# Kernel tuning notes

Measured on AMD Instinct MI355X. Metric: run time of the kernel, lower is better.

## Reference

```python
import jax, jax.numpy as jnp
import numpy as np

B, N, D, H, NW = 16, 400, 256, 8, 4
DH = D // H
EPS_LN = 1e-5

def _layer_norm(x, g, b):
    m = jnp.mean(x, axis=-1, keepdims=True)
    v = jnp.mean((x - m) ** 2, axis=-1, keepdims=True)
    return (x - m) / jnp.sqrt(v + EPS_LN) * g + b

def setup_inputs() -> dict:
    key = jax.random.key(0)
    ks = jax.random.split(key, 10)
    p = lambda k, shape: (jax.random.normal(k, shape, jnp.float32) * 0.02)
    return {
        'x': jax.random.normal(ks[0], (B, N, D), jnp.float32),
        'attention_weights': jax.random.normal(ks[1], (B, NW, N, N), jnp.float32),
        'Wq': p(ks[2], (D, D)), 'bq': jnp.zeros((D,), jnp.float32),
        'Wk': p(ks[3], (D, D)), 'bk': jnp.zeros((D,), jnp.float32),
        'Wv': p(ks[4], (D, D)), 'bv': jnp.zeros((D,), jnp.float32),
        'Wo': p(ks[5], (D, D)), 'bo': jnp.zeros((D,), jnp.float32),
        'g1': jnp.ones((D,), jnp.float32), 'beta1': jnp.zeros((D,), jnp.float32),
        'W1': p(ks[6], (4 * D, D)), 'b1': jnp.zeros((4 * D,), jnp.float32),
        'W2': p(ks[7], (D, 4 * D)), 'b2': jnp.zeros((D,), jnp.float32),
        'g2': jnp.ones((D,), jnp.float32), 'beta2': jnp.zeros((D,), jnp.float32),
    }

def reference(x, attention_weights, Wq, bq, Wk, bk, Wv, bv, Wo, bo,
              g1, beta1, W1, b1, W2, b2, g2, beta2):
    b, n, d = x.shape
    # QKV projections, split heads: [B, H, N, DH]
    q = (x @ Wq.T + bq).reshape(b, n, H, DH).transpose(0, 2, 1, 3)
    k = (x @ Wk.T + bk).reshape(b, n, H, DH).transpose(0, 2, 1, 3)
    v = (x @ Wv.T + bv).reshape(b, n, H, DH).transpose(0, 2, 1, 3)
    qk = jnp.einsum('bhnd,bhmd->bhnm', q, k) / np.sqrt(DH)  # [B,H,N,N]
    # signed attention averaged over the NW per-sample weight matrices
    nw = attention_weights.shape[1]
    scores = jnp.zeros_like(qk)
    for i in range(nw):  # small fixed count, not a data dim
        w = attention_weights[:, i][:, None, :, :]  # [B,1,N,N]
        s = qk * w
        e = jnp.exp(jnp.abs(s))
        scores = scores + jnp.sign(s) * e / (jnp.sum(e, axis=-1, keepdims=True) + 1e-10)
    scores = scores / nw
    attn_out = jnp.einsum('bhnm,bhmd->bhnd', scores, v)
    attn_out = attn_out.transpose(0, 2, 1, 3).reshape(b, n, d)
    attn_out = attn_out @ Wo.T + bo
    h = _layer_norm(x + attn_out, g1, beta1)
    ffn = jax.nn.relu(h @ W1.T + b1) @ W2.T + b2
    y = _layer_norm(h + ffn, g2, beta2)
    return (y, scores)
```

## Files before the change

kernel.cpp:

```cpp
#include <hip/hip_runtime.h>
#include <hip/hip_fp16.h>

typedef unsigned int uint32;

#define B_ 16
#define N_ 400
#define D_ 256
#define H_ 8
#define DH_ 32
#define NW_ 4

#if __has_builtin(__builtin_amdgcn_exp2f)
#define EXP2(x) __builtin_amdgcn_exp2f(x)
#else
#define EXP2(x) exp2f(x)
#endif

#define QK_SCL 0.2550348f

using bf16x8 = __attribute__((ext_vector_type(8))) short;
using f16x8  = __attribute__((ext_vector_type(8))) _Float16;
using f16x4  = __attribute__((ext_vector_type(4))) _Float16;
using f32x4  = __attribute__((ext_vector_type(4))) float;

__device__ __forceinline__ ushort f2b(float f) {
  uint32 u = __float_as_uint(f);
  uint32 r = (u + 0x7fffu + ((u >> 16) & 1u)) >> 16;
  return (ushort)r;
}

__global__ __launch_bounds__(256) void convert_kernel(
    const float* __restrict__ x,  const float* __restrict__ wq,
    const float* __restrict__ wk, const float* __restrict__ wv,
    const float* __restrict__ wo, const float* __restrict__ w1,
    const float* __restrict__ w2,
    ushort* __restrict__ xb,  ushort* __restrict__ wqb,
    ushort* __restrict__ wkb, ushort* __restrict__ wvb,
    ushort* __restrict__ wob, ushort* __restrict__ w1b,
    ushort* __restrict__ w2b) {
  int gid = blockIdx.x * 256 + threadIdx.x;
  const float* src; ushort* dst;
  if      (gid < 409600) { src = x;  dst = xb;  }
  else if ((gid -= 409600) < 16384) { src = wq; dst = wqb; }
  else if ((gid -= 16384) < 16384)  { src = wk; dst = wkb; }
  else if ((gid -= 16384) < 16384)  { src = wv; dst = wvb; }
  else if ((gid -= 16384) < 16384)  { src = wo; dst = wob; }
  else if ((gid -= 16384) < 65536)  { src = w1; dst = w1b; }
  else { gid -= 65536; src = w2; dst = w2b; }
  float4 f = ((const float4*)src)[gid];
  ushort4 u;
  u.x = f2b(f.x); u.y = f2b(f.y); u.z = f2b(f.z); u.w = f2b(f.w);
  *(ushort4*)&dst[(size_t)gid * 4] = u;
}

template <int RELU, int RESID, int OUT_F32, int OUT_BF16>
__global__ __launch_bounds__(256) void gemm_bt(
    const ushort* __restrict__ A, const ushort* __restrict__ W,
    const float* __restrict__ bias, const float* __restrict__ resid,
    float* __restrict__ outf, ushort* __restrict__ outb,
    int M, int N, int K) {
  __shared__ __align__(16) ushort As[2][64 * 40];
  __shared__ __align__(16) ushort Ws[2][64 * 40];
  int t = threadIdx.x;
  int l = t & 63, w = t >> 6;
  int n0 = blockIdx.x * 64, m0 = blockIdx.y * 64;
  int srow = t >> 2, sc = (t & 3) * 8;
  int lrow = l & 15, lk = (l >> 4) * 8;

  const uint4* ag = (const uint4*)&A[(size_t)(m0 + srow) * K + sc];
  const uint4* wg = (const uint4*)&W[(size_t)(n0 + srow) * K + sc];
  uint4 ar = ag[0], wr = wg[0];
  int nk = K >> 5;

  f32x4 acc[4];
#pragma unroll
  for (int nt = 0; nt < 4; nt++) acc[nt] = {0.f, 0.f, 0.f, 0.f};

  for (int kk = 0; kk < nk; kk++) {
    int cur = kk & 1;
    *(uint4*)&As[cur][srow * 40 + sc] = ar;
    *(uint4*)&Ws[cur][srow * 40 + sc] = wr;
    if (kk + 1 < nk) { ar = ag[(size_t)(kk + 1) * 4]; wr = wg[(size_t)(kk + 1) * 4]; }
    __syncthreads();
    bf16x8 af = *(const bf16x8*)&As[cur][(16 * w + lrow) * 40 + lk];
#pragma unroll
    for (int nt = 0; nt < 4; nt++) {
      bf16x8 bf = *(const bf16x8*)&Ws[cur][(nt * 16 + lrow) * 40 + lk];
      acc[nt] = __builtin_amdgcn_mfma_f32_16x16x32_bf16(af, bf, acc[nt], 0, 0, 0);
    }
  }

#pragma unroll
  for (int nt = 0; nt < 4; nt++) {
    int n = n0 + nt * 16 + lrow;
    float bv = bias[n];
#pragma unroll
    for (int r = 0; r < 4; r++) {
      int m = m0 + 16 * w + (l >> 4) * 4 + r;
      float v = acc[nt][r] + bv;
      if (RELU)  v = fmaxf(v, 0.f);
      if (RESID) v += resid[(size_t)m * N + n];
      if (OUT_F32)  outf[(size_t)m * N + n] = v;
      if (OUT_BF16) outb[(size_t)m * N + n] = f2b(v);
    }
  }
}

__global__ __launch_bounds__(256) void qkv_gemm(
    const ushort* __restrict__ xb, const ushort* __restrict__ wq,
    const ushort* __restrict__ wk, const ushort* __restrict__ wv,
    const float* __restrict__ bq, const float* __restrict__ bk,
    const float* __restrict__ bv,
    _Float16* __restrict__ qh, _Float16* __restrict__ kh,
    _Float16* __restrict__ vt) {
  __shared__ __align__(16) ushort As[2][64 * 40];
  __shared__ __align__(16) ushort Ws[2][64 * 40];
  int z = blockIdx.z;
  const ushort* W = (z == 0) ? wq : (z == 1) ? wk : wv;
  const float* bias = (z == 0) ? bq : (z == 1) ? bk : bv;

  int t = threadIdx.x;
  int l = t & 63, w = t >> 6;
  int n0 = blockIdx.x * 64, m0 = blockIdx.y * 64;
  int srow = t >> 2, sc = (t & 3) * 8;
  int lrow = l & 15, lk = (l >> 4) * 8;

  const uint4* ag = (const uint4*)&xb[(size_t)(m0 + srow) * 256 + sc];
  const uint4* wg = (const uint4*)&W[(size_t)(n0 + srow) * 256 + sc];
  uint4 ar = ag[0], wr = wg[0];

  f32x4 acc[4];
#pragma unroll
  for (int nt = 0; nt < 4; nt++) acc[nt] = {0.f, 0.f, 0.f, 0.f};

  for (int kk = 0; kk < 8; kk++) {
    int cur = kk & 1;
    *(uint4*)&As[cur][srow * 40 + sc] = ar;
    *(uint4*)&Ws[cur][srow * 40 + sc] = wr;
    if (kk + 1 < 8) { ar = ag[(kk + 1) * 4]; wr = wg[(kk + 1) * 4]; }
    __syncthreads();
    bf16x8 af = *(const bf16x8*)&As[cur][(16 * w + lrow) * 40 + lk];
#pragma unroll
    for (int nt = 0; nt < 4; nt++) {
      bf16x8 bf = *(const bf16x8*)&Ws[cur][(nt * 16 + lrow) * 40 + lk];
      acc[nt] = __builtin_amdgcn_mfma_f32_16x16x32_bf16(af, bf, acc[nt], 0, 0, 0);
    }
  }

  int mb = m0 + 16 * w + (l >> 4) * 4;
  int bb = mb / 400;
  int mi = mb - bb * 400;
#pragma unroll
  for (int nt = 0; nt < 4; nt++) {
    int n = n0 + nt * 16 + lrow;
    float bvv = bias[n];
    if (z < 2) {
      _Float16* out = z ? kh : qh;
      float scl = z ? 1.f : QK_SCL;
      int hh = n >> 5, dd = n & 31;
      _Float16* dst = out + (((size_t)(bb * 8 + hh)) * 400 + mi) * 32 + dd;
#pragma unroll
      for (int r = 0; r < 4; r++)
        dst[(size_t)r * 32] = (_Float16)((acc[nt][r] + bvv) * scl);
    } else {
      _Float16 h4[4];
#pragma unroll
      for (int r = 0; r < 4; r++) h4[r] = (_Float16)(acc[nt][r] + bvv);
      *(uint2*)&vt[((size_t)bb * 256 + n) * 400 + mi] = *(uint2*)h4;
    }
  }
}

#define SP 416

__global__ __launch_bounds__(256) void attn_kernel(
    const _Float16* __restrict__ qh, const _Float16* __restrict__ kh,
    const _Float16* __restrict__ vt, const float* __restrict__ aw,
    float* __restrict__ scores, ushort* __restrict__ attnb) {
  __shared__ __align__(16) char smem[16 * SP * 2];
  __half* S = (__half*)smem;

  int id = blockIdx.x;
  int c = ((id >> 6) << 3) | (id & 7);
  int hh = (id >> 3) & 7;
  int b = c / 25;
  int n0 = (c - b * 25) * 16;

  int t = threadIdx.x;
  int w = t >> 6, l = t & 63;
  int lq = l >> 4, lr = l & 15;

  {
    const _Float16* qbase = qh + (((size_t)(b * 8 + hh)) * 400 + n0) * 32;
    const _Float16* kbase = kh + ((size_t)(b * 8 + hh)) * 400 * 32;
    f16x8 af = *(const f16x8*)(qbase + lr * 32 + lq * 8);
    for (int mt = w; mt < 25; mt += 4) {
      f16x8 bf = *(const f16x8*)(kbase + (size_t)(mt * 16 + lr) * 32 + lq * 8);
      f32x4 cc = {0.f, 0.f, 0.f, 0.f};
      cc = __builtin_amdgcn_mfma_f32_16x16x32_f16(af, bf, cc, 0, 0, 0);
#pragma unroll
      for (int r = 0; r < 4; r++)
        S[(lq * 4 + r) * SP + mt * 16 + lr] = __float2half(cc[r]);
    }
  }
  __syncthreads();

  {
    _Float16* Sh16 = (_Float16*)S;
    const float* awb = aw + (((size_t)(b * 4)) * 400 + n0) * 400;
    float* scb = scores + (((size_t)(b * 8 + hh)) * 400 + n0) * 400;
    int m0 = l * 4, m1 = 256 + l * 4;
    bool act = (l < 36);
#pragma unroll 1
    for (int nn = 0; nn < 4; nn++) {
      int n = w * 4 + nn;
      _Float16* srow = Sh16 + (size_t)n * SP;
      f16x4 s0 = *(const f16x4*)(srow + m0);
      f16x4 s1; s1[0] = s1[1] = s1[2] = s1[3] = (_Float16)0.f;
      if (act) s1 = *(const f16x4*)(srow + m1);
      float q0[4], q1[4];
#pragma unroll
      for (int j = 0; j < 4; j++) { q0[j] = (float)s0[j]; q1[j] = (float)s1[j]; }
      f16x4 e0[4], e1[4];
      float zinv[4];
#pragma unroll
      for (int i = 0; i < 4; i++) {
        const float* awn = awb + (size_t)i * 160000 + (size_t)n * 400;
        float4 a0 = *(const float4*)(awn + m0);
        float z = 0.f;
#pragma unroll
        for (int j = 0; j < 4; j++) {
          float tt = q0[j] * ((const float*)&a0)[j];
          float ef = EXP2(fabsf(tt));
          z += ef;
          e0[i][j] = (_Float16)copysignf(ef, tt);
        }
        if (act) {
          float4 a1 = *(const float4*)(awn + m1);
#pragma unroll
          for (int j = 0; j < 4; j++) {
            float tt = q1[j] * ((const float*)&a1)[j];
            float ef = EXP2(fabsf(tt));
            z += ef;
            e1[i][j] = (_Float16)copysignf(ef, tt);
          }
        } else {
          e1[i][0] = e1[i][1] = e1[i][2] = e1[i][3] = (_Float16)0.f;
        }
        z += __shfl_xor(z, 1);
        z += __shfl_xor(z, 2);
        z += __shfl_xor(z, 4);
        z += __shfl_xor(z, 8);
        z += __shfl_xor(z, 16);
        z += __shfl_xor(z, 32);
        zinv[i] = 0.25f / (z + 1e-10f);
      }
      float o0[4] = {0.f, 0.f, 0.f, 0.f}, o1[4] = {0.f, 0.f, 0.f, 0.f};
#pragma unroll
      for (int i = 0; i < 4; i++) {
#pragma unroll
        for (int j = 0; j < 4; j++) {
          o0[j] += (float)e0[i][j] * zinv[i];
          o1[j] += (float)e1[i][j] * zinv[i];
        }
      }
      float* scout = scb + (size_t)n * 400;
      *(float4*)(scout + m0) = *(float4*)o0;
      f16x4 h0;
#pragma unroll
      for (int j = 0; j < 4; j++) h0[j] = (_Float16)o0[j];
      *(f16x4*)(srow + m0) = h0;
      if (act) {
        *(float4*)(scout + m1) = *(float4*)o1;
        f16x4 h1;
#pragma unroll
        for (int j = 0; j < 4; j++) h1[j] = (_Float16)o1[j];
        *(f16x4*)(srow + m1) = h1;
      } else if (l < 40) {
        f16x4 hz; hz[0] = hz[1] = hz[2] = hz[3] = (_Float16)0.f;
        *(f16x4*)(srow + m1) = hz;
      }
    }
  }
  __syncthreads();

  const _Float16* vbase = vt + (((size_t)b) * 256 + hh * 32) * 400;
  f32x4 a0 = {0.f, 0.f, 0.f, 0.f}, a1 = {0.f, 0.f, 0.f, 0.f};
  const _Float16* Sh = (const _Float16*)S;
  for (int c2 = w; c2 < 13; c2 += 4) {
    f16x8 sf = *(const f16x8*)(Sh + lr * SP + c2 * 32 + lq * 8);
    f16x8 v0 = *(const f16x8*)(vbase + (size_t)lr * 400 + c2 * 32 + lq * 8);
    f16x8 v1 = *(const f16x8*)(vbase + (size_t)(16 + lr) * 400 + c2 * 32 + lq * 8);
    a0 = __builtin_amdgcn_mfma_f32_16x16x32_f16(sf, v0, a0, 0, 0, 0);
    a1 = __builtin_amdgcn_mfma_f32_16x16x32_f16(sf, v1, a1, 0, 0, 0);
  }
  __syncthreads();
  float* Of = (float*)smem;
#pragma unroll
  for (int r = 0; r < 4; r++) {
    Of[(w * 16 + lq * 4 + r) * 32 + lr] = a0[r];
    Of[(w * 16 + lq * 4 + r) * 32 + 16 + lr] = a1[r];
  }
  __syncthreads();
  for (int o = t; o < 512; o += 256) {
    int n = o >> 5, d = o & 31;
    float s = Of[n * 32 + d] + Of[512 + n * 32 + d] +
              Of[1024 + n * 32 + d] + Of[1536 + n * 32 + d];
    attnb[((size_t)(b * 400 + n0 + n)) * 256 + hh * 32 + d] = f2b(s);
  }
}

__global__ __launch_bounds__(256) void ln_kernel(
    const float* __restrict__ src, const float* __restrict__ g,
    const float* __restrict__ be, float* __restrict__ outf,
    ushort* __restrict__ outb) {
  int row = blockIdx.x, t = threadIdx.x;
  float v = src[(size_t)row * 256 + t];
  __shared__ float red[4];
  float s = v;
#pragma unroll
  for (int o = 32; o > 0; o >>= 1) s += __shfl_down(s, o, 64);
  if ((t & 63) == 0) red[t >> 6] = s;
  __syncthreads();
  float mean = (red[0] + red[1] + red[2] + red[3]) * (1.f / 256.f);
  __syncthreads();
  float d = v - mean;
  s = d * d;
#pragma unroll
  for (int o = 32; o > 0; o >>= 1) s += __shfl_down(s, o, 64);
  if ((t & 63) == 0) red[t >> 6] = s;
  __syncthreads();
  float var = (red[0] + red[1] + red[2] + red[3]) * (1.f / 256.f);
  float y = d * rsqrtf(var + 1e-5f) * g[t] + be[t];
  outf[(size_t)row * 256 + t] = y;
  if (outb) outb[(size_t)row * 256 + t] = f2b(y);
}

extern "C" void kernel_launch(void* const* d_in, const int* in_sizes, int n_in,
                              void* d_out, int out_size, void* d_ws,
                              size_t ws_size, hipStream_t stream) {
  const float* x   = (const float*)d_in[0];
  const float* aw  = (const float*)d_in[1];
  const float* Wq  = (const float*)d_in[2];
  const float* bq  = (const float*)d_in[3];
  const float* Wk  = (const float*)d_in[4];
  const float* bk  = (const float*)d_in[5];
  const float* Wv  = (const float*)d_in[6];
  const float* bv  = (const float*)d_in[7];
  const float* Wo  = (const float*)d_in[8];
  const float* bo  = (const float*)d_in[9];
  const float* g1  = (const float*)d_in[10];
  const float* be1 = (const float*)d_in[11];
  const float* W1  = (const float*)d_in[12];
  const float* b1  = (const float*)d_in[13];
  const float* W2  = (const float*)d_in[14];
  const float* b2  = (const float*)d_in[15];
  const float* g2  = (const float*)d_in[16];
  const float* be2 = (const float*)d_in[17];

  if (ws_size < 34340864) return;

  char* ws = (char*)d_ws;
  ushort*   xb    = (ushort*)(ws + 0);
  ushort*   wqb   = (ushort*)(ws + 3276800);
  ushort*   wkb   = (ushort*)(ws + 3407872);
  ushort*   wvb   = (ushort*)(ws + 3538944);
  ushort*   wob   = (ushort*)(ws + 3670016);
  ushort*   w1b   = (ushort*)(ws + 3801088);
  ushort*   w2b   = (ushort*)(ws + 4325376);
  _Float16* qhb   = (_Float16*)(ws + 4849664);
  _Float16* khb   = (_Float16*)(ws + 8126464);
  _Float16* vtb   = (_Float16*)(ws + 11403264);
  ushort*   attnb = (ushort*)(ws + 14680064);
  float*    ao    = (float*)(ws + 17956864);
  float*    hbuf  = (float*)(ws + 24510464);
  ushort*   hb    = (ushort*)(ws + 31064064);
  ushort*   ffn1b = (ushort*)qhb;
  float*    ffn2  = ao;

  float* yout   = (float*)d_out;
  float* scores = yout + 1638400;

  convert_kernel<<<2368, 256, 0, stream>>>(x, Wq, Wk, Wv, Wo, W1, W2,
                                           xb, wqb, wkb, wvb, wob, w1b, w2b);
  qkv_gemm<<<dim3(4, 100, 3), 256, 0, stream>>>(
      xb, wqb, wkb, wvb, bq, bk, bv, qhb, khb, vtb);
  attn_kernel<<<3200, 256, 0, stream>>>(qhb, khb, vtb, aw, scores, attnb);
  gemm_bt<0, 1, 1, 0><<<dim3(4, 100), 256, 0, stream>>>(
      attnb, wob, bo, x, ao, nullptr, 6400, 256, 256);
  ln_kernel<<<6400, 256, 0, stream>>>(ao, g1, be1, hbuf, hb);
  gemm_bt<1, 0, 0, 1><<<dim3(16, 100), 256, 0, stream>>>(
      hb, w1b, b1, nullptr, nullptr, ffn1b, 6400, 1024, 256);
  gemm_bt<0, 1, 1, 0><<<dim3(4, 100), 256, 0, stream>>>(
      ffn1b, w2b, b2, hbuf, ffn2, nullptr, 6400, 256, 1024);
  ln_kernel<<<6400, 256, 0, stream>>>(ffn2, g2, be2, yout, nullptr);
}
```

Baseline: 283.1 us.

## Use 512-thread attention blocks with one half-wavefront per score row

The attention kernel now launches 512 threads per block. In the signed-softmax phase, each group of 32 lanes owns one of the 16 query rows and all four weight matrices at once, replacing the old loop where each wave processed four rows in sequence. The four row sums are reduced together through 5-step shuffles, and the MFMA and output-reduction loops are respread over 8 waves. This adds parallelism and memory-level concurrency for the bandwidth-heavy aw and scores traffic. In exchange it uses more registers per thread and leaves some waves idle in the small MFMA loops.

```diff
diff --git a/kernel.cpp b/kernel.cpp
--- a/kernel.cpp
+++ b/kernel.cpp
@@ -173,11 +173,11 @@
 
 #define SP 416
 
-__global__ __launch_bounds__(256) void attn_kernel(
+__global__ __launch_bounds__(512) void attn_kernel(
     const _Float16* __restrict__ qh, const _Float16* __restrict__ kh,
     const _Float16* __restrict__ vt, const float* __restrict__ aw,
     float* __restrict__ scores, ushort* __restrict__ attnb) {
-  __shared__ __align__(16) char smem[16 * SP * 2];
+  __shared__ __align__(16) char smem[16384];
   __half* S = (__half*)smem;
 
   int id = blockIdx.x;
@@ -194,7 +194,7 @@
     const _Float16* qbase = qh + (((size_t)(b * 8 + hh)) * 400 + n0) * 32;
     const _Float16* kbase = kh + ((size_t)(b * 8 + hh)) * 400 * 32;
     f16x8 af = *(const f16x8*)(qbase + lr * 32 + lq * 8);
-    for (int mt = w; mt < 25; mt += 4) {
+    for (int mt = w; mt < 25; mt += 8) {
       f16x8 bf = *(const f16x8*)(kbase + (size_t)(mt * 16 + lr) * 32 + lq * 8);
       f32x4 cc = {0.f, 0.f, 0.f, 0.f};
       cc = __builtin_amdgcn_mfma_f32_16x16x32_f16(af, bf, cc, 0, 0, 0);
@@ -206,79 +206,89 @@
   __syncthreads();
 
   {
-    _Float16* Sh16 = (_Float16*)S;
-    const float* awb = aw + (((size_t)(b * 4)) * 400 + n0) * 400;
-    float* scb = scores + (((size_t)(b * 8 + hh)) * 400 + n0) * 400;
-    int m0 = l * 4, m1 = 256 + l * 4;
-    bool act = (l < 36);
-#pragma unroll 1
-    for (int nn = 0; nn < 4; nn++) {
-      int n = w * 4 + nn;
-      _Float16* srow = Sh16 + (size_t)n * SP;
-      f16x4 s0 = *(const f16x4*)(srow + m0);
-      f16x4 s1; s1[0] = s1[1] = s1[2] = s1[3] = (_Float16)0.f;
-      if (act) s1 = *(const f16x4*)(srow + m1);
-      float q0[4], q1[4];
-#pragma unroll
-      for (int j = 0; j < 4; j++) { q0[j] = (float)s0[j]; q1[j] = (float)s1[j]; }
-      f16x4 e0[4], e1[4];
-      float zinv[4];
-#pragma unroll
-      for (int i = 0; i < 4; i++) {
-        const float* awn = awb + (size_t)i * 160000 + (size_t)n * 400;
-        float4 a0 = *(const float4*)(awn + m0);
-        float z = 0.f;
+    int n = t >> 5, p = t & 31;
+    _Float16* srow = (_Float16*)S + (size_t)n * SP;
+    const float* awn = aw + (((size_t)(b * 4)) * 400 + n0 + n) * 400;
+    float* scout = scores + (((size_t)(b * 8 + hh)) * 400 + n0 + n) * 400;
+    int mB = p * 4;
+    bool act3 = (p < 4);
+
+    float q[4][4];
+#pragma unroll
+    for (int k = 0; k < 3; k++) {
+      f16x4 s = *(const f16x4*)(srow + mB + 128 * k);
+#pragma unroll
+      for (int j = 0; j < 4; j++) q[k][j] = (float)s[j];
+    }
+    if (act3) {
+      f16x4 s = *(const f16x4*)(srow + mB + 384);
+#pragma unroll
+      for (int j = 0; j < 4; j++) q[3][j] = (float)s[j];
+    } else {
+#pragma unroll
+      for (int j = 0; j < 4; j++) q[3][j] = 0.f;
+    }
+
+    f16x4 e[4][4];
+    float z[4];
+#pragma unroll
+    for (int i = 0; i < 4; i++) {
+      const float* awi = awn + (size_t)i * 160000;
+      float zz = 0.f;
+#pragma unroll
+      for (int k = 0; k < 3; k++) {
+        float4 a = *(const float4*)(awi + mB + 128 * k);
 #pragma unroll
         for (int j = 0; j < 4; j++) {
-          float tt = q0[j] * ((const float*)&a0)[j];
+          float tt = q[k][j] * ((const float*)&a)[j];
           float ef = EXP2(fabsf(tt));
-          z += ef;
-          e0[i][j] = (_Float16)copysignf(ef, tt);
-        }
-        if (act) {
-          float4 a1 = *(const float4*)(awn + m1);
-#pragma unroll
-          for (int j = 0; j < 4; j++) {
-            float tt = q1[j] * ((const float*)&a1)[j];
-            float ef = EXP2(fabsf(tt));
-            z += ef;
-            e1[i][j] = (_Float16)copysignf(ef, tt);
-          }
-        } else {
-          e1[i][0] = e1[i][1] = e1[i][2] = e1[i][3] = (_Float16)0.f;
-        }
-        z += __shfl_xor(z, 1);
-        z += __shfl_xor(z, 2);
-        z += __shfl_xor(z, 4);
-        z += __shfl_xor(z, 8);
-        z += __shfl_xor(z, 16);
-        z += __shfl_xor(z, 32);
-        zinv[i] = 0.25f / (z + 1e-10f);
-      }
-      float o0[4] = {0.f, 0.f, 0.f, 0.f}, o1[4] = {0.f, 0.f, 0.f, 0.f};
-#pragma unroll
-      for (int i = 0; i < 4; i++) {
-#pragma unroll
-        for (int j = 0; j < 4; j++) {
-          o0[j] += (float)e0[i][j] * zinv[i];
-          o1[j] += (float)e1[i][j] * zinv[i];
+          zz += ef;
+          e[i][k][j] = (_Float16)copysignf(ef, tt);
         }
       }
-      float* scout = scb + (size_t)n * 400;
-      *(float4*)(scout + m0) = *(float4*)o0;
-      f16x4 h0;
-#pragma unroll
-      for (int j = 0; j < 4; j++) h0[j] = (_Float16)o0[j];
-      *(f16x4*)(srow + m0) = h0;
-      if (act) {
-        *(float4*)(scout + m1) = *(float4*)o1;
-        f16x4 h1;
-#pragma unroll
-        for (int j = 0; j < 4; j++) h1[j] = (_Float16)o1[j];
-        *(f16x4*)(srow + m1) = h1;
-      } else if (l < 40) {
-        f16x4 hz; hz[0] = hz[1] = hz[2] = hz[3] = (_Float16)0.f;
-        *(f16x4*)(srow + m1) = hz;
+      if (act3) {
+        float4 a = *(const float4*)(awi + mB + 384);
+#pragma unroll
+        for (int j = 0; j < 4; j++) {
+          float tt = q[3][j] * ((const float*)&a)[j];
+          float ef = EXP2(fabsf(tt));
+          zz += ef;
+          e[i][3][j] = (_Float16)copysignf(ef, tt);
+        }
+      } else {
+#pragma unroll
+        for (int j = 0; j < 4; j++) e[i][3][j] = (_Float16)0.f;
+      }
+      z[i] = zz;
+    }
+
+#pragma unroll
+    for (int o = 1; o <= 16; o <<= 1) {
+#pragma unroll
+      for (int i = 0; i < 4; i++) z[i] += __shfl_xor(z[i], o);
+    }
+    float zinv[4];
+#pragma unroll
+    for (int i = 0; i < 4; i++) zinv[i] = 0.25f / (z[i] + 1e-10f);
+
+#pragma unroll
+    for (int k = 0; k < 4; k++) {
+      float o4[4] = {0.f, 0.f, 0.f, 0.f};
+#pragma unroll
+      for (int i = 0; i < 4; i++)
+#pragma unroll
+        for (int j = 0; j < 4; j++)
+          o4[j] += (float)e[i][k][j] * zinv[i];
+      f16x4 h;
+#pragma unroll
+      for (int j = 0; j < 4; j++) h[j] = (_Float16)o4[j];
+      float4 ov = {o4[0], o4[1], o4[2], o4[3]};
+      if (k < 3) {
+        *(f16x4*)(srow + mB + 128 * k) = h;
+        *(float4*)(scout + mB + 128 * k) = ov;
+      } else {
+        if (p < 8) *(f16x4*)(srow + mB + 384) = h;
+        if (act3)  *(float4*)(scout + mB + 384) = ov;
       }
     }
   }
@@ -287,7 +297,7 @@
   const _Float16* vbase = vt + (((size_t)b) * 256 + hh * 32) * 400;
   f32x4 a0 = {0.f, 0.f, 0.f, 0.f}, a1 = {0.f, 0.f, 0.f, 0.f};
   const _Float16* Sh = (const _Float16*)S;
-  for (int c2 = w; c2 < 13; c2 += 4) {
+  for (int c2 = w; c2 < 13; c2 += 8) {
     f16x8 sf = *(const f16x8*)(Sh + lr * SP + c2 * 32 + lq * 8);
     f16x8 v0 = *(const f16x8*)(vbase + (size_t)lr * 400 + c2 * 32 + lq * 8);
     f16x8 v1 = *(const f16x8*)(vbase + (size_t)(16 + lr) * 400 + c2 * 32 + lq * 8);
@@ -302,10 +312,11 @@
     Of[(w * 16 + lq * 4 + r) * 32 + 16 + lr] = a1[r];
   }
   __syncthreads();
-  for (int o = t; o < 512; o += 256) {
-    int n = o >> 5, d = o & 31;
-    float s = Of[n * 32 + d] + Of[512 + n * 32 + d] +
-              Of[1024 + n * 32 + d] + Of[1536 + n * 32 + d];
+  {
+    int n = t >> 5, d = t & 31;
+    float s = 0.f;
+#pragma unroll
+    for (int ww = 0; ww < 8; ww++) s += Of[ww * 512 + n * 32 + d];
     attnb[((size_t)(b * 400 + n0 + n)) * 256 + hh * 32 + d] = f2b(s);
   }
 }
@@ -385,7 +396,7 @@
                                            xb, wqb, wkb, wvb, wob, w1b, w2b);
   qkv_gemm<<<dim3(4, 100, 3), 256, 0, stream>>>(
       xb, wqb, wkb, wvb, bq, bk, bv, qhb, khb, vtb);
-  attn_kernel<<<3200, 256, 0, stream>>>(qhb, khb, vtb, aw, scores, attnb);
+  attn_kernel<<<3200, 512, 0, stream>>>(qhb, khb, vtb, aw, scores, attnb);
   gemm_bt<0, 1, 1, 0><<<dim3(4, 100), 256, 0, stream>>>(
       attnb, wob, bo, x, ao, nullptr, 6400, 256, 256);
   ln_kernel<<<6400, 256, 0, stream>>>(ao, g1, be1, hbuf, hb);
```

After: 296.4 us. 4.7% more time.

## Batch softmax shuffles, accumulate in fp16, raise attn occupancy hint

Applied to the files above, without the earlier changes.

Adds a minimum-blocks-per-CU hint to the attention kernel so the compiler limits registers and allows more resident waves. Interleaves the rows each wave processes, and batches the four per-weight normalizer reductions so their shuffles are issued together instead of serially. Accumulates the weighted sum of the four exponential terms in packed fp16 vector math rather than fp32. The fp16 accumulation lowers precision of the stored scores output, and the register cap may cause spilling.

```diff
diff --git a/kernel.cpp b/kernel.cpp
--- a/kernel.cpp
+++ b/kernel.cpp
@@ -173,7 +173,7 @@
 
 #define SP 416
 
-__global__ __launch_bounds__(256) void attn_kernel(
+__global__ __launch_bounds__(256, 8) void attn_kernel(
     const _Float16* __restrict__ qh, const _Float16* __restrict__ kh,
     const _Float16* __restrict__ vt, const float* __restrict__ aw,
     float* __restrict__ scores, ushort* __restrict__ attnb) {
@@ -206,78 +206,92 @@
   __syncthreads();
 
   {
-    _Float16* Sh16 = (_Float16*)S;
+    int m0 = l * 4, m1 = 256 + l * 4;
+    bool act = (l < 36);
     const float* awb = aw + (((size_t)(b * 4)) * 400 + n0) * 400;
     float* scb = scores + (((size_t)(b * 8 + hh)) * 400 + n0) * 400;
-    int m0 = l * 4, m1 = 256 + l * 4;
-    bool act = (l < 36);
 #pragma unroll 1
-    for (int nn = 0; nn < 4; nn++) {
-      int n = w * 4 + nn;
-      _Float16* srow = Sh16 + (size_t)n * SP;
+    for (int g = 0; g < 4; g++) {
+      int n = g * 4 + w;
+      _Float16* srow = (_Float16*)S + (size_t)n * SP;
+      const float* awn = awb + (size_t)n * 400;
+      float* scout = scb + (size_t)n * 400;
+
       f16x4 s0 = *(const f16x4*)(srow + m0);
-      f16x4 s1; s1[0] = s1[1] = s1[2] = s1[3] = (_Float16)0.f;
-      if (act) s1 = *(const f16x4*)(srow + m1);
       float q0[4], q1[4];
 #pragma unroll
-      for (int j = 0; j < 4; j++) { q0[j] = (float)s0[j]; q1[j] = (float)s1[j]; }
+      for (int j = 0; j < 4; j++) q0[j] = (float)s0[j];
+      if (act) {
+        f16x4 s1 = *(const f16x4*)(srow + m1);
+#pragma unroll
+        for (int j = 0; j < 4; j++) q1[j] = (float)s1[j];
+      } else {
+#pragma unroll
+        for (int j = 0; j < 4; j++) q1[j] = 0.f;
+      }
+
       f16x4 e0[4], e1[4];
-      float zinv[4];
+      float z[4];
 #pragma unroll
       for (int i = 0; i < 4; i++) {
-        const float* awn = awb + (size_t)i * 160000 + (size_t)n * 400;
-        float4 a0 = *(const float4*)(awn + m0);
-        float z = 0.f;
+        const float* awi = awn + (size_t)i * 160000;
+        float4 a0 = *(const float4*)(awi + m0);
+        float zz = 0.f;
 #pragma unroll
         for (int j = 0; j < 4; j++) {
           float tt = q0[j] * ((const float*)&a0)[j];
           float ef = EXP2(fabsf(tt));
-          z += ef;
+          zz += ef;
           e0[i][j] = (_Float16)copysignf(ef, tt);
         }
         if (act) {
-          float4 a1 = *(const float4*)(awn + m1);
+          float4 a1 = *(const float4*)(awi + m1);
 #pragma unroll
           for (int j = 0; j < 4; j++) {
             float tt = q1[j] * ((const float*)&a1)[j];
             float ef = EXP2(fabsf(tt));
-            z += ef;
+            zz += ef;
             e1[i][j] = (_Float16)copysignf(ef, tt);
           }
         } else {
-          e1[i][0] = e1[i][1] = e1[i][2] = e1[i][3] = (_Float16)0.f;
+#pragma unroll
+          for (int j = 0; j < 4; j++) e1[i][j] = (_Float16)0.f;
         }
-        z += __shfl_xor(z, 1);
-        z += __shfl_xor(z, 2);
-        z += __shfl_xor(z, 4);
-        z += __shfl_xor(z, 8);
-        z += __shfl_xor(z, 16);
-        z += __shfl_xor(z, 32);
-        zinv[i] = 0.25f / (z + 1e-10f);
+        z[i] = zz;
       }
-      float o0[4] = {0.f, 0.f, 0.f, 0.f}, o1[4] = {0.f, 0.f, 0.f, 0.f};
+
+#pragma unroll
+      for (int o = 1; o <= 32; o <<= 1) {
+#pragma unroll
+        for (int i = 0; i < 4; i++) z[i] += __shfl_xor(z[i], o);
+      }
+
+      f16x4 o0, o1;
+#pragma unroll
+      for (int j = 0; j < 4; j++) { o0[j] = (_Float16)0.f; o1[j] = (_Float16)0.f; }
 #pragma unroll
       for (int i = 0; i < 4; i++) {
-#pragma unroll
-        for (int j = 0; j < 4; j++) {
-          o0[j] += (float)e0[i][j] * zinv[i];
-          o1[j] += (float)e1[i][j] * zinv[i];
-        }
+        _Float16 zh = (_Float16)(0.25f / (z[i] + 1e-10f));
+        f16x4 zv = {zh, zh, zh, zh};
+        o0 += e0[i] * zv;
+        o1 += e1[i] * zv;
       }
-      float* scout = scb + (size_t)n * 400;
-      *(float4*)(scout + m0) = *(float4*)o0;
-      f16x4 h0;
-#pragma unroll
-      for (int j = 0; j < 4; j++) h0[j] = (_Float16)o0[j];
-      *(f16x4*)(srow + m0) = h0;
+
+      float4 so;
+#pragma unroll
+      for (int j = 0; j < 4; j++) ((float*)&so)[j] = (float)o0[j];
+      *(float4*)(scout + m0) = so;
+      *(f16x4*)(srow + m0) = o0;
       if (act) {
-        *(float4*)(scout + m1) = *(float4*)o1;
-        f16x4 h1;
-#pragma unroll
-        for (int j = 0; j < 4; j++) h1[j] = (_Float16)o1[j];
-        *(f16x4*)(srow + m1) = h1;
+        float4 s1o;
+#pragma unroll
+        for (int j = 0; j < 4; j++) ((float*)&s1o)[j] = (float)o1[j];
+        *(float4*)(scout + m1) = s1o;
+        *(f16x4*)(srow + m1) = o1;
       } else if (l < 40) {
-        f16x4 hz; hz[0] = hz[1] = hz[2] = hz[3] = (_Float16)0.f;
+        f16x4 hz;
+#pragma unroll
+        for (int j = 0; j < 4; j++) hz[j] = (_Float16)0.f;
         *(f16x4*)(srow + m1) = hz;
       }
     }
```

Result: faster. 276.1 us (-2.5%).
